# Optimization experiments

Measured on AMD Instinct MI355X. Metric: run time of the kernel, lower is better.

The kernel has to match this reference:

```python
import jax, jax.numpy as jnp
import numpy as np

B, N, DY, STD, T = 2, 8000, 12, 6, 30
DX = 0.5
DYG = 0.5
DT = 1.0

def _mlp(x, params):
    n = len(params)
    for i, (W, b) in enumerate(params):
        x = x @ W + b
        if i < n - 1:
            x = jax.nn.relu(x)
    return x

def _process_param(D, mu, coeff_vec):
    ds = DY // 3
    d33 = ds * ds
    m33 = [coeff_vec[i * d33:(i + 1) * d33].reshape(ds, ds) for i in range(4)]
    base = 4 * d33
    dd = ds * ds - ds
    diag = []
    for i in range(3):
        aij = coeff_vec[base + i * dd:base + (i + 1) * dd].reshape(ds - 1, ds)
        m = jnp.concatenate([jnp.ones((ds - 1, 1), aij.dtype), aij], axis=1).reshape(-1)
        m = jnp.concatenate([m, jnp.ones((1,), aij.dtype)]).reshape(ds, ds)
        diag.append(m)
    z = jnp.zeros((ds, ds), coeff_vec.dtype)
    rows = jnp.concatenate([
        jnp.concatenate([diag[0], z, m33[0]], axis=1),
        jnp.concatenate([z, diag[1], m33[1]], axis=1),
        jnp.concatenate([m33[2], m33[3], diag[2]], axis=1)], axis=0)
    coeffM = jax.nn.relu(rows)  # [DY, DY]
    ds0 = jnp.zeros((ds,), D.dtype)
    Dij = jax.nn.relu(jnp.concatenate([ds0, D]))  # [DY]
    MUij = jax.nn.relu(jnp.concatenate([mu[:ds], ds0, mu[-ds:]]))  # [DY]
    return coeffM, Dij, MUij

def _overlap(t, g):
    # overlap length of unit intervals centered at t and g
    omin = jax.nn.relu((t - 0.5) - (g - 0.5)) + (g - 0.5)
    omax = (t + 0.5) - jax.nn.relu((t + 0.5) - (g + 0.5))
    return jax.nn.relu(omax - omin)

def _trans_probs(dx_, dy_):
    gx, gy = jnp.meshgrid(jnp.arange(5.0), jnp.arange(5.0), indexing='ij')
    grid = jnp.stack([gx, gy], -1).reshape(25, 2)
    xl = _overlap(dx_[..., None, :], grid[:, 1].reshape(1, 1, 25, 1))
    yl = _overlap(dy_[..., None, :], grid[:, 0].reshape(1, 1, 25, 1))
    return xl * yl  # [B,N,25,C]

def _aggre(inp, a0):
    x = inp[:, a0]  # [B,N,25,C] gather
    w = jnp.concatenate([jnp.ones((1,)), jnp.full((24,), 0.01)]).reshape(1, 1, 25, 1)
    return jnp.concatenate([inp, (x * w).sum(-2)], axis=-1)

def _pde(phi, feat_dy, feat_st, D, mu, coeff_vec, trans_p, q_p, dec_p, adj4, adj25, ckpt=False):
    a4 = adj4[0]   # [N,4]
    a0 = adj25[0]  # [N,25]
    coeffM, Dij, MUij = _process_param(D, mu, coeff_vec)
    phie = phi[..., None]
    pn = phie[:, a4]  # [B,N,4,1]
    gpx = (pn[:, :, 1] - pn[:, :, 0]) / (2 * DX)
    gpy = (pn[:, :, 3] - pn[:, :, 2]) / (2 * DYG)
    phi_ag = _aggre(phie, a0)      # constant across steps
    st_ag = _aggre(feat_st, a0)    # constant across steps
    D_bn = jnp.broadcast_to(jax.lax.stop_gradient(Dij), (B, N, DY))
    MU_bn = jnp.broadcast_to(jax.lax.stop_gradient(MUij), (B, N, DY))

    def step(feat, _):
        last = feat
        fn = feat[:, a4]  # [B,N,4,C]
        J = (fn[:, :, 0] + fn[:, :, 1] - 2 * feat) / DX ** 2 + (fn[:, :, 2] + fn[:, :, 3] - 2 * feat) / DYG ** 2
        fxn = (gpx * feat)[:, a4]
        fyn = (gpy * feat)[:, a4]
        Fdiv = (fxn[:, :, 1] - fxn[:, :, 0]) / (2 * DX) + (fyn[:, :, 3] - fyn[:, :, 2]) / (2 * DYG)
        u_diff = jnp.einsum('bnc,cd->bnd', Dij * J - MUij * Fdiv, coeffM)
        mass = jnp.where(last == 0, 1.0, last)
        a_x = jnp.clip(jnp.einsum('bnc,cd->bnd', MUij * gpx, coeffM) / mass, -2.0, 2.0)
        a_y = jnp.clip(jnp.einsum('bnc,cd->bnd', MUij * gpy, coeffM) / mass, -2.0, 2.0)
        probs = _trans_probs(a_x * DT, a_y * DT)  # [B,N,25,C]
        src = probs * last[:, :, None, :]
        scat = lambda idx, s: jnp.zeros((N, DY), s.dtype).at[idx.reshape(-1)].add(s.reshape(-1, DY))
        u_rig = jax.vmap(scat)(adj25, src) - last  # scatter_add over nodes then sum over 25
        feat_tr = jnp.concatenate([_aggre(feat, a0), phi_ag, D_bn, MU_bn, st_ag], -1)  # [B,N,62]
        mix = jax.nn.sigmoid(_mlp(feat_tr, trans_p)[..., -1:])
        delta_u = mix * u_diff + (1 - mix) * u_rig
        feat_q = jnp.concatenate([_aggre(last, a0), phi_ag, st_ag], -1)  # [B,N,38]
        q0 = _mlp(feat_q, q_p)
        new = last + delta_u + q0
        fu = _mlp(jnp.concatenate([new, feat_st], -1), dec_p)  # [B,N,1]
        return new, (fu[..., 0], mix[..., 0], q0, new)

    body = jax.checkpoint(step) if ckpt else step
    _, (us_s, mix_s, q0_s, fd_s) = jax.lax.scan(body, feat_dy, None, length=T)
    us = jnp.moveaxis(us_s, 0, -1).reshape(B, N, 1, T)
    mix_m = jnp.moveaxis(mix_s, 0, -1).reshape(B, N, 1, T)
    q0_m = jnp.moveaxis(q0_s, 0, -1).reshape(B, N, DY, 1, T)
    fd = jnp.moveaxis(fd_s, 0, 2).reshape(B, N, 1, T, DY)
    return us, mix_m, q0_m, fd

def setup_inputs():
    key = jax.random.key(0)
    ks = jax.random.split(key, 24)
    def lin(k, i, o):
        kw, kb = jax.random.split(k)
        return (0.1 * jax.random.normal(kw, (i, o), jnp.float32),
                0.01 * jax.random.normal(kb, (o,), jnp.float32))
    tp = [lin(ks[0], 62, 64), lin(ks[1], 64, 32), lin(ks[2], 32, 26)]
    qp = [lin(ks[3], 38, 64), lin(ks[4], 64, 32), lin(ks[5], 32, 12)]
    dp = [lin(ks[6], 18, 32), lin(ks[7], 32, 32), lin(ks[8], 32, 64), lin(ks[9], 64, 1)]
    inp = {
        'phi': jax.random.normal(ks[10], (B, N), jnp.float32),
        'feat_dy': jax.random.uniform(ks[11], (B, N, DY), jnp.float32),
        'feat_st': jax.random.normal(ks[12], (B, N, STD), jnp.float32),
        'D': jnp.ones((2 * (DY // 3),), jnp.float32) * 0.05,
        'mu': jnp.ones((2 * (DY // 3),), jnp.float32) * 0.05,
        'coeff_vec': jnp.ones((DY * DY - 2 * (DY // 3) ** 2 - DY,), jnp.float32) * 0.05,
        'adj4': jax.random.randint(ks[13], (B, N, 4), 0, N),
        'adj25': jax.random.randint(ks[14], (B, N, 25), 0, N),
    }
    for name, p in [('trans', tp), ('q', qp), ('dec', dp)]:
        for i, (W, b) in enumerate(p):
            inp[name + '_W' + str(i)] = W
            inp[name + '_b' + str(i)] = b
    return inp

def reference(phi, feat_dy, feat_st, D, mu, coeff_vec,
              trans_W0, trans_b0, trans_W1, trans_b1, trans_W2, trans_b2,
              q_W0, q_b0, q_W1, q_b1, q_W2, q_b2,
              dec_W0, dec_b0, dec_W1, dec_b1, dec_W2, dec_b2, dec_W3, dec_b3,
              adj4, adj25):
    trans_p = [(trans_W0, trans_b0), (trans_W1, trans_b1), (trans_W2, trans_b2)]
    q_p = [(q_W0, q_b0), (q_W1, q_b1), (q_W2, q_b2)]
    dec_p = [(dec_W0, dec_b0), (dec_W1, dec_b1), (dec_W2, dec_b2), (dec_W3, dec_b3)]
    return _pde(phi, feat_dy, feat_st, D, mu, coeff_vec, trans_p, q_p, dec_p, adj4, adj25)
```

## Files before the change

### kernel.cpp

```cpp
#include <hip/hip_runtime.h>
#include <math.h>


namespace {
constexpr int NB = 2;
constexpr int NN = 8000;
constexpr int BN = NB * NN;
constexpr int TS = 30;
constexpr int CAP = 64;

constexpr int P_T0 = 0;
constexpr int P_Q0 = 1536;
constexpr int P_W1 = 3072;
constexpr int P_Q2 = 7168;
constexpr int P_Z  = 7552;
constexpr int P_D0 = 7584;
constexpr int P_D1 = 7968;
constexpr int P_D2 = 8992;
constexpr int P_D3 = 11040;
constexpr int P_BT1 = 11104;
constexpr int P_BQ1 = 11136;
constexpr int P_BQ2 = 11168;
constexpr int P_BD1 = 11184;
constexpr int P_BD2 = 11216;
constexpr int P_MISC= 11280;
constexpr int PACK_N = 11296;

constexpr int A_AG = 0;
constexpr int A_NV = 0;
constexpr int A_H1 = 24;
constexpr int A_D1 = 24;
constexpr int A_D2 = 56;
constexpr int A_H2 = 152;
constexpr int A_SLOT = 216;

constexpr int O_COEFF = 0;
constexpr int O_CFT   = 144;
constexpr int O_DIJ   = 288;
constexpr int O_MUIJ  = 300;
constexpr int O_MC    = 312;
constexpr int O_PACK  = 336;
constexpr int O_GPX   = O_PACK + PACK_N + 16;
constexpr int O_GPY   = O_GPX + BN;
constexpr int O_H1T   = O_GPY + BN;
constexpr int O_H1Q   = O_H1T + BN*64;
constexpr int O_H1D   = O_H1Q + BN*64;
constexpr int O_FEATA = O_H1D + BN*32;
constexpr int O_FEATB = O_FEATA + BN*12;
constexpr int O_AXY4A = O_FEATB + BN*12;
constexpr int O_AXY4B = O_AXY4A + BN*48;
constexpr int O_ACT   = O_AXY4B + BN*48;
constexpr int O_FLTEND= O_ACT + BN*48;
constexpr int O_STG   = O_FLTEND + BN + BN*CAP;
constexpr int STG_N = TS*BN*12;
constexpr size_t WS_NEED = (size_t)(O_STG + STG_N) * 4;

constexpr int OUS  = 0;
constexpr int OMIX = BN*TS;
constexpr int OQ0  = 2*BN*TS;
constexpr int OFD  = OQ0 + BN*12*TS;
}

__device__ __forceinline__ float group5_sum(float v, int lane) {
  int g = lane / 12, c = lane % 12;
  float s1 = __shfl(v, c + 12*((g+1)%5));
  float s2 = __shfl(v, c + 12*((g+2)%5));
  float s3 = __shfl(v, c + 12*((g+3)%5));
  float s4 = __shfl(v, c + 12*((g+4)%5));
  return v + s1 + s2 + s3 + s4;
}

__global__ void k_setup_small(const float* __restrict__ D, const float* __restrict__ mu,
                              const float* __restrict__ cv, float* ws) {
  int t = threadIdx.x;
  for (int e = t; e < 144; e += 256) {
    int r = e / 12, q = e % 12;
    int rb = r >> 2, cb = q >> 2, ri = r & 3, qi = q & 3;
    float val = 0.f;
    if (rb == cb) {
      int f = ri*4 + qi;
      if (f % 5 == 0) val = 1.f;
      else val = cv[64 + rb*12 + (f/5)*4 + (f%5) - 1];
    } else if (rb == 0 && cb == 2) val = cv[     ri*4 + qi];
    else if   (rb == 1 && cb == 2) val = cv[16 + ri*4 + qi];
    else if   (rb == 2 && cb == 0) val = cv[32 + ri*4 + qi];
    else if   (rb == 2 && cb == 1) val = cv[48 + ri*4 + qi];
    ws[O_COEFF + e] = fmaxf(val, 0.f);
  }
  if (t < 12) {
    ws[O_DIJ + t]  = (t < 4) ? 0.f : fmaxf(D[t-4], 0.f);
    ws[O_MUIJ + t] = (t < 4) ? fmaxf(mu[t], 0.f) : ((t < 8) ? 0.f : fmaxf(mu[t-4], 0.f));
  }
  __syncthreads();
  if (t < 144) {
    int r = t / 12, c = t % 12;
    ws[O_CFT + c*12 + r] = ws[O_COEFF + t];
  }
  if (t < 12) {
    float acc = 0.f;
    for (int c = 0; c < 12; c++) acc += ws[O_MUIJ + c] * ws[O_COEFF + c*12 + t];
    ws[O_MC + t] = acc;
  }
}

__global__ void k_xpose(const float* __restrict__ Wt0, const float* __restrict__ Wq0,
                        const float* __restrict__ Wt1, const float* __restrict__ Wq1,
                        const float* __restrict__ Wt2, const float* __restrict__ Wq2,
                        const float* __restrict__ Wd0, const float* __restrict__ Wd1,
                        const float* __restrict__ Wd2, const float* __restrict__ Wd3,
                        const float* __restrict__ bt1, const float* __restrict__ bq1,
                        const float* __restrict__ bt2, const float* __restrict__ bq2,
                        const float* __restrict__ bd1, const float* __restrict__ bd2,
                        const float* __restrict__ bd3,
                        float* ws) {
  const int t = blockIdx.x * blockDim.x + threadIdx.x;
  const int G = gridDim.x * blockDim.x;
  float* P = ws + O_PACK;
  for (int e = t; e < 1536; e += G) {
    int q = e / 256, r = e % 256, l = r / 4, j = r % 4;
    P[P_T0 + e] = Wt0[(4*q+j)*64 + l];
    P[P_Q0 + e] = Wq0[(4*q+j)*64 + l];
  }
  for (int e = t; e < 4096; e += G) {
    int q = e / 256, r = e % 256, l = r / 4, j = r % 4;
    P[P_W1 + e] = (l < 32) ? Wt1[(4*q+j)*32 + l] : Wq1[(4*q+j)*32 + (l-32)];
  }
  for (int e = t; e < 384; e += G) {
    int q = e / 48, r = e % 48, c = r / 4, j = r % 4;
    P[P_Q2 + e] = Wq2[(4*q+j)*12 + c];
  }
  for (int e = t; e < 32; e += G) P[P_Z + e] = Wt2[e*26 + 25];
  for (int e = t; e < 384; e += G) {
    int q = e / 128, r = e % 128, l = r / 4, j = r % 4;
    P[P_D0 + e] = Wd0[(4*q+j)*32 + l];
  }
  for (int e = t; e < 1024; e += G) {
    int q = e / 128, r = e % 128, l = r / 4, j = r % 4;
    P[P_D1 + e] = Wd1[(4*q+j)*32 + l];
  }
  for (int e = t; e < 2048; e += G) {
    int q = e / 256, r = e % 256, l = r / 4, j = r % 4;
    P[P_D2 + e] = Wd2[(4*q+j)*64 + l];
  }
  for (int e = t; e < 64; e += G) P[P_D3 + e] = Wd3[e];
  for (int e = t; e < 32; e += G) {
    P[P_BT1 + e] = bt1[e];
    P[P_BQ1 + e] = bq1[e];
    P[P_BD1 + e] = bd1[e];
  }
  for (int e = t; e < 12; e += G) P[P_BQ2 + e] = bq2[e];
  for (int e = t; e < 64; e += G) P[P_BD2 + e] = bd2[e];
  if (t == 0) { P[P_MISC + 0] = bd3[0]; P[P_MISC + 1] = bt2[25]; }
}

__global__ __launch_bounds__(256) void k_setup_node(
    const float* __restrict__ phi, const float* __restrict__ feat_dy,
    const float* __restrict__ feat_st,
    const int* __restrict__ adj4, const int* __restrict__ adj25,
    const float* __restrict__ Wt0, const float* __restrict__ bt0,
    const float* __restrict__ Wq0, const float* __restrict__ bq0,
    const float* __restrict__ Wd0, const float* __restrict__ bd0,
    float* ws, int* wsi) {
  const int wid  = (blockIdx.x * blockDim.x + threadIdx.x) >> 6;
  const int lane = threadIdx.x & 63;
  if (wid >= BN) return;
  const int b = wid / NN, n = wid % NN;

  const int* a4 = adj4 + n*4;
  const float gpx = phi[b*NN + a4[1]] - phi[b*NN + a4[0]];
  const float gpy = phi[b*NN + a4[3]] - phi[b*NN + a4[2]];
  if (lane == 0) { ws[O_GPX + wid] = gpx; ws[O_GPY + wid] = gpy; wsi[wid] = 0; }

  int idx = 0; float w = 0.f;
  if (lane < 25) { idx = adj25[n*25 + lane]; w = (lane == 0) ? 1.f : 0.01f; }
  float phiw = (lane < 25) ? w * phi[b*NN + idx] : 0.f;
  #pragma unroll
  for (int s = 32; s > 0; s >>= 1) phiw += __shfl_xor(phiw, s);

  float stv[6], stw[6];
  #pragma unroll
  for (int j = 0; j < 6; j++) {
    float x = (lane < 25) ? w * feat_st[(b*NN + idx)*6 + j] : 0.f;
    #pragma unroll
    for (int s = 32; s > 0; s >>= 1) x += __shfl_xor(x, s);
    stw[j] = x;
    stv[j] = feat_st[(b*NN + n)*6 + j];
  }
  const float phiv = phi[b*NN + n];

  float hT = bt0[lane] + phiv*Wt0[24*64 + lane] + phiw*Wt0[25*64 + lane];
  float hQ = bq0[lane] + phiv*Wq0[24*64 + lane] + phiw*Wq0[25*64 + lane];
  #pragma unroll
  for (int i = 0; i < 12; i++) {
    hT = fmaf(ws[O_DIJ  + i], Wt0[(26+i)*64 + lane], hT);
    hT = fmaf(ws[O_MUIJ + i], Wt0[(38+i)*64 + lane], hT);
  }
  #pragma unroll
  for (int j = 0; j < 6; j++) {
    hT = fmaf(stv[j], Wt0[(50+j)*64 + lane], hT);
    hT = fmaf(stw[j], Wt0[(56+j)*64 + lane], hT);
    hQ = fmaf(stv[j], Wq0[(26+j)*64 + lane], hQ);
    hQ = fmaf(stw[j], Wq0[(32+j)*64 + lane], hQ);
  }
  ws[O_H1T + wid*64 + lane] = hT;
  ws[O_H1Q + wid*64 + lane] = hQ;
  if (lane < 32) {
    float hD = bd0[lane];
    #pragma unroll
    for (int j = 0; j < 6; j++) hD = fmaf(stv[j], Wd0[(12+j)*32 + lane], hD);
    ws[O_H1D + wid*32 + lane] = hD;
  }
  if (lane < 12) {
    float f = feat_dy[wid*12 + lane];
    ws[O_FEATA + wid*12 + lane] = f;
    float mass = (f == 0.f) ? 1.f : f;
    float mc = ws[O_MC + lane];
    float axv = fminf(fmaxf(gpx*mc/mass, -2.f), 2.f);
    float ayv = fminf(fmaxf(gpy*mc/mass, -2.f), 2.f);
    float4* a4a = (float4*)(ws + O_AXY4A);
    a4a[wid*12 + lane] = make_float4(f, axv, ayv, 0.f);
  }
}

__global__ void k_build_rev(const int* __restrict__ adj25, int* wsi) {
  int i = blockIdx.x * blockDim.x + threadIdx.x;
  if (i >= BN * 25) return;
  int b = i / (NN * 25);
  int rem = i % (NN * 25);
  int m = rem / 25, k = rem % 25;
  int tgt = adj25[i];
  int slot = atomicAdd(&wsi[b*NN + tgt], 1);
  if (slot < CAP) wsi[BN + (b*NN + tgt)*CAP + slot] = (m << 5) | k;
}

__global__ __launch_bounds__(512) void k_gather(
    const float* __restrict__ ws,
    const int* __restrict__ rcnt, const int* __restrict__ rent,
    const float* __restrict__ fsrc, const float4* __restrict__ a4src,
    const int* __restrict__ adj4, const int* __restrict__ adj25,
    float* __restrict__ actb) {
  const int wid_raw = (int)((blockIdx.x * blockDim.x + threadIdx.x) >> 6);
  if (wid_raw >= BN) return;
  const int wid  = __builtin_amdgcn_readfirstlane(wid_raw);
  const int lane = threadIdx.x & 63;
  const int c12  = lane % 12;
  const int g    = lane / 12;
  const int b = wid / NN, n = wid % NN;

  const int* a4p = adj4 + n*4;
  const int m0 = a4p[0], m1 = a4p[1], m2 = a4p[2], m3 = a4p[3];
  int cnt = rcnt[wid]; if (cnt > CAP) cnt = CAP;
  const int idxv = (lane < 25) ? adj25[n*25 + lane] : 0;
  const int pkv  = rent[wid*CAP + lane];
  const float f_c  = fsrc[wid*12 + c12];
  const float dij  = ws[O_DIJ  + c12];
  const float muij = ws[O_MUIJ + c12];
  const float4* CFTp = (const float4*)(ws + O_CFT + c12*12);
  const float4 cf0 = CFTp[0], cf1 = CFTp[1], cf2 = CFTp[2];

  float agw = 0.f;
  {
    const int i0 = __shfl(idxv, g);
    const int i1 = __shfl(idxv, g + 5);
    const int i2 = __shfl(idxv, g + 10);
    const int i3 = __shfl(idxv, g + 15);
    const int i4 = __shfl(idxv, g + 20);
    if (g < 5) {
      const float v0 = fsrc[(b*NN + i0)*12 + c12];
      const float v1 = fsrc[(b*NN + i1)*12 + c12];
      const float v2 = fsrc[(b*NN + i2)*12 + c12];
      const float v3 = fsrc[(b*NN + i3)*12 + c12];
      const float v4 = fsrc[(b*NN + i4)*12 + c12];
      const float w0 = (g == 0) ? 1.f : 0.01f;
      agw = fmaf(w0,    v0, agw);
      agw = fmaf(0.01f, v1, agw);
      agw = fmaf(0.01f, v2, agw);
      agw = fmaf(0.01f, v3, agw);
      agw = fmaf(0.01f, v4, agw);
    }
    agw = group5_sum(agw, lane);
  }

  float udiff;
  {
    const float f0 = fsrc[(b*NN+m0)*12 + c12];
    const float f1 = fsrc[(b*NN+m1)*12 + c12];
    const float f2 = fsrc[(b*NN+m2)*12 + c12];
    const float f3 = fsrc[(b*NN+m3)*12 + c12];
    const float gx0 = ws[O_GPX + b*NN + m0], gx1 = ws[O_GPX + b*NN + m1];
    const float gy2 = ws[O_GPY + b*NN + m2], gy3 = ws[O_GPY + b*NN + m3];
    const float J = 4.f * ((f0+f1+f2+f3) - 4.f*f_c);
    const float Fdiv = gx1*f1 - gx0*f0 + gy3*f3 - gy2*f2;
    const float v = dij*J - muij*Fdiv;
    float acc;
    acc  = __shfl(v, 0) * cf0.x;
    acc  = fmaf(__shfl(v, 1), cf0.y, acc);
    acc  = fmaf(__shfl(v, 2), cf0.z, acc);
    acc  = fmaf(__shfl(v, 3), cf0.w, acc);
    acc  = fmaf(__shfl(v, 4), cf1.x, acc);
    acc  = fmaf(__shfl(v, 5), cf1.y, acc);
    acc  = fmaf(__shfl(v, 6), cf1.z, acc);
    acc  = fmaf(__shfl(v, 7), cf1.w, acc);
    acc  = fmaf(__shfl(v, 8), cf2.x, acc);
    acc  = fmaf(__shfl(v, 9), cf2.y, acc);
    acc  = fmaf(__shfl(v,10), cf2.z, acc);
    acc  = fmaf(__shfl(v,11), cf2.w, acc);
    udiff = acc;
  }

  float urig;
  {
    float usc = 0.f;
    #pragma unroll
    for (int it = 0; it < 8; ++it) {
      const int e = g + 5*it;
      const bool val = (g < 5) && (e < cnt);
      const int pk = __shfl(pkv, e & 63);
      const int m = pk >> 5, k = pk & 31;
      const int off = val ? ((b*NN + m)*12 + c12) : (wid*12 + c12);
      const float4 sm = a4src[off];
      const float kx = (float)(k - (k/5)*5);
      const float ky = (float)(k/5);
      const float px = fmaxf(1.f - fabsf(sm.y - kx), 0.f);
      const float py = fmaxf(1.f - fabsf(sm.z - ky), 0.f);
      usc = fmaf(val ? px*py : 0.f, sm.x, usc);
    }
    if (cnt > 40) {
      #pragma unroll
      for (int it = 8; it < 13; ++it) {
        const int e = g + 5*it;
        const bool val = (g < 5) && (e < cnt);
        const int pk = __shfl(pkv, e & 63);
        const int m = pk >> 5, k = pk & 31;
        const int off = val ? ((b*NN + m)*12 + c12) : (wid*12 + c12);
        const float4 sm = a4src[off];
        const float kx = (float)(k - (k/5)*5);
        const float ky = (float)(k/5);
        const float px = fmaxf(1.f - fabsf(sm.y - kx), 0.f);
        const float py = fmaxf(1.f - fabsf(sm.z - ky), 0.f);
        usc = fmaf(val ? px*py : 0.f, sm.x, usc);
      }
    }
    usc = group5_sum(usc, lane);
    urig = usc - f_c;
  }

  const float ov = (lane < 12) ? agw : ((lane < 24) ? udiff : urig);
  if (lane < 36) actb[wid*48 + lane] = ov;
}

__global__ __launch_bounds__(512) void k_mlp(
    const float* __restrict__ ws, const float* __restrict__ actb, int t,
    const float* __restrict__ fsrc,
    float* __restrict__ fdst, float4* __restrict__ a4dst,
    float* __restrict__ stg, int use_stage,
    float* __restrict__ out) {
  __shared__ __attribute__((aligned(16))) float sh[PACK_N + 16*A_SLOT];
  const int tid = threadIdx.x;
  {
    const float4* wp = (const float4*)(ws + O_PACK);
    float4* sp = (float4*)sh;
    for (int e = tid; e < PACK_N/4; e += 512) sp[e] = wp[e];
  }
  __syncthreads();

  const int wv   = tid >> 6;
  const int wvq  = __builtin_amdgcn_readfirstlane(wv);
  const int lane = tid & 63;
  const int c12 = lane % 12;
  const int l32 = lane & 31;
  const bool isQ = lane >= 32;
  float* act0 = sh + PACK_N + (wvq*2 + 0)*A_SLOT;
  float* act1 = sh + PACK_N + (wvq*2 + 1)*A_SLOT;

  const float mcv = ws[O_MC + c12];

  #pragma unroll 1
  for (int pass = 0; pass < 2; pass++) {
    const int nb = (blockIdx.x*16 + pass*8 + wvq) * 2;

    float f_c[2], udiff[2], urig[2];
    #pragma unroll
    for (int j = 0; j < 2; j++) {
      const int wid = nb + j;
      float* actj = j ? act1 : act0;
      f_c[j] = fsrc[wid*12 + c12];
      const float agv = actb[wid*48 + c12];
      udiff[j] = actb[wid*48 + 12 + c12];
      urig[j]  = actb[wid*48 + 24 + c12];
      if (lane < 24) actj[A_AG + lane] = (lane < 12) ? f_c[j] : agv;
    }

    {
      float h1t0 = ws[O_H1T + nb*64 + lane];
      float h1q0 = ws[O_H1Q + nb*64 + lane];
      float h1t1 = ws[O_H1T + (nb+1)*64 + lane];
      float h1q1 = ws[O_H1Q + (nb+1)*64 + lane];
      #pragma unroll
      for (int q = 0; q < 6; q++) {
        const float4 wt = *(const float4*)&sh[P_T0 + q*256 + lane*4];
        const float4 wq = *(const float4*)&sh[P_Q0 + q*256 + lane*4];
        const float4 a0 = *(const float4*)&act0[A_AG + 4*q];
        const float4 a1 = *(const float4*)&act1[A_AG + 4*q];
        h1t0 = fmaf(a0.x, wt.x, h1t0); h1q0 = fmaf(a0.x, wq.x, h1q0);
        h1t0 = fmaf(a0.y, wt.y, h1t0); h1q0 = fmaf(a0.y, wq.y, h1q0);
        h1t0 = fmaf(a0.z, wt.z, h1t0); h1q0 = fmaf(a0.z, wq.z, h1q0);
        h1t0 = fmaf(a0.w, wt.w, h1t0); h1q0 = fmaf(a0.w, wq.w, h1q0);
        h1t1 = fmaf(a1.x, wt.x, h1t1); h1q1 = fmaf(a1.x, wq.x, h1q1);
        h1t1 = fmaf(a1.y, wt.y, h1t1); h1q1 = fmaf(a1.y, wq.y, h1q1);
        h1t1 = fmaf(a1.z, wt.z, h1t1); h1q1 = fmaf(a1.z, wq.z, h1q1);
        h1t1 = fmaf(a1.w, wt.w, h1t1); h1q1 = fmaf(a1.w, wq.w, h1q1);
      }
      act0[A_H1 + lane]      = fmaxf(h1t0, 0.f);
      act0[A_H1 + 64 + lane] = fmaxf(h1q0, 0.f);
      act1[A_H1 + lane]      = fmaxf(h1t1, 0.f);
      act1[A_H1 + 64 + lane] = fmaxf(h1q1, 0.f);
    }

    {
      const int hoff = isQ ? 64 : 0;
      float h2_0 = isQ ? sh[P_BQ1 + l32] : sh[P_BT1 + l32];
      float h2_1 = h2_0;
      #pragma unroll
      for (int q = 0; q < 16; q++) {
        const float4 w  = *(const float4*)&sh[P_W1 + q*256 + lane*4];
        const float4 a0 = *(const float4*)&act0[A_H1 + hoff + 4*q];
        const float4 a1 = *(const float4*)&act1[A_H1 + hoff + 4*q];
        h2_0 = fmaf(a0.x, w.x, h2_0); h2_1 = fmaf(a1.x, w.x, h2_1);
        h2_0 = fmaf(a0.y, w.y, h2_0); h2_1 = fmaf(a1.y, w.y, h2_1);
        h2_0 = fmaf(a0.z, w.z, h2_0); h2_1 = fmaf(a1.z, w.z, h2_1);
        h2_0 = fmaf(a0.w, w.w, h2_0); h2_1 = fmaf(a1.w, w.w, h2_1);
      }
      act0[A_H2 + lane] = fmaxf(h2_0, 0.f);
      act1[A_H2 + lane] = fmaxf(h2_1, 0.f);
    }

    float mix[2], q0v[2];
    {
      float mz0 = sh[P_MISC + 1], mz1 = mz0;
      float q00 = sh[P_BQ2 + c12], q01 = q00;
      #pragma unroll
      for (int q = 0; q < 8; q++) {
        const float4 wz  = *(const float4*)&sh[P_Z + 4*q];
        const float4 wq  = *(const float4*)&sh[P_Q2 + q*48 + c12*4];
        const float4 at0 = *(const float4*)&act0[A_H2 + 4*q];
        const float4 aq0 = *(const float4*)&act0[A_H2 + 32 + 4*q];
        const float4 at1 = *(const float4*)&act1[A_H2 + 4*q];
        const float4 aq1 = *(const float4*)&act1[A_H2 + 32 + 4*q];
        mz0 = fmaf(at0.x, wz.x, mz0); q00 = fmaf(aq0.x, wq.x, q00);
        mz0 = fmaf(at0.y, wz.y, mz0); q00 = fmaf(aq0.y, wq.y, q00);
        mz0 = fmaf(at0.z, wz.z, mz0); q00 = fmaf(aq0.z, wq.z, q00);
        mz0 = fmaf(at0.w, wz.w, mz0); q00 = fmaf(aq0.w, wq.w, q00);
        mz1 = fmaf(at1.x, wz.x, mz1); q01 = fmaf(aq1.x, wq.x, q01);
        mz1 = fmaf(at1.y, wz.y, mz1); q01 = fmaf(aq1.y, wq.y, q01);
        mz1 = fmaf(at1.z, wz.z, mz1); q01 = fmaf(aq1.z, wq.z, q01);
        mz1 = fmaf(at1.w, wz.w, mz1); q01 = fmaf(aq1.w, wq.w, q01);
      }
      mix[0] = 1.f / (1.f + expf(-mz0));
      mix[1] = 1.f / (1.f + expf(-mz1));
      q0v[0] = q00; q0v[1] = q01;
    }

    #pragma unroll
    for (int j = 0; j < 2; j++) {
      const int wid = nb + j;
      float* actj = j ? act1 : act0;
      const float newv = f_c[j] + mix[j]*udiff[j] + (1.f - mix[j])*urig[j] + q0v[j];
      if (lane < 12) {
        actj[A_NV + lane] = newv;
        if (use_stage) stg[(size_t)t*BN*12 + wid*12 + lane] = q0v[j];
        else           out[OQ0 + (wid*12 + lane)*TS + t] = q0v[j];
        out[OFD + (wid*TS + t)*12 + lane] = newv;
        fdst[wid*12 + lane] = newv;
        float mass = (newv == 0.f) ? 1.f : newv;
        float gpxn = ws[O_GPX + wid], gpyn = ws[O_GPY + wid];
        float axn = fminf(fmaxf(gpxn*mcv/mass, -2.f), 2.f);
        float ayn = fminf(fmaxf(gpyn*mcv/mass, -2.f), 2.f);
        a4dst[wid*12 + lane] = make_float4(newv, axn, ayn, 0.f);
      }
      if (lane == 0) out[OMIX + wid*TS + t] = mix[j];
    }

    {
      float d1_0 = ws[O_H1D + nb*32 + l32];
      float d1_1 = ws[O_H1D + (nb+1)*32 + l32];
      #pragma unroll
      for (int q = 0; q < 3; q++) {
        const float4 w  = *(const float4*)&sh[P_D0 + q*128 + l32*4];
        const float4 a0 = *(const float4*)&act0[A_NV + 4*q];
        const float4 a1 = *(const float4*)&act1[A_NV + 4*q];
        d1_0 = fmaf(a0.x, w.x, d1_0); d1_1 = fmaf(a1.x, w.x, d1_1);
        d1_0 = fmaf(a0.y, w.y, d1_0); d1_1 = fmaf(a1.y, w.y, d1_1);
        d1_0 = fmaf(a0.z, w.z, d1_0); d1_1 = fmaf(a1.z, w.z, d1_1);
        d1_0 = fmaf(a0.w, w.w, d1_0); d1_1 = fmaf(a1.w, w.w, d1_1);
      }
      if (lane < 32) {
        act0[A_D1 + lane] = fmaxf(d1_0, 0.f);
        act1[A_D1 + lane] = fmaxf(d1_1, 0.f);
      }
    }
    {
      float d2_0 = sh[P_BD1 + l32], d2_1 = d2_0;
      #pragma unroll
      for (int q = 0; q < 8; q++) {
        const float4 w  = *(const float4*)&sh[P_D1 + q*128 + l32*4];
        const float4 a0 = *(const float4*)&act0[A_D1 + 4*q];
        const float4 a1 = *(const float4*)&act1[A_D1 + 4*q];
        d2_0 = fmaf(a0.x, w.x, d2_0); d2_1 = fmaf(a1.x, w.x, d2_1);
        d2_0 = fmaf(a0.y, w.y, d2_0); d2_1 = fmaf(a1.y, w.y, d2_1);
        d2_0 = fmaf(a0.z, w.z, d2_0); d2_1 = fmaf(a1.z, w.z, d2_1);
        d2_0 = fmaf(a0.w, w.w, d2_0); d2_1 = fmaf(a1.w, w.w, d2_1);
      }
      if (lane < 32) {
        act0[A_D2 + lane] = fmaxf(d2_0, 0.f);
        act1[A_D2 + lane] = fmaxf(d2_1, 0.f);
      }
    }
    {
      float d3_0 = sh[P_BD2 + lane], d3_1 = d3_0;
      #pragma unroll
      for (int q = 0; q < 8; q++) {
        const float4 w  = *(const float4*)&sh[P_D2 + q*256 + lane*4];
        const float4 a0 = *(const float4*)&act0[A_D2 + 4*q];
        const float4 a1 = *(const float4*)&act1[A_D2 + 4*q];
        d3_0 = fmaf(a0.x, w.x, d3_0); d3_1 = fmaf(a1.x, w.x, d3_1);
        d3_0 = fmaf(a0.y, w.y, d3_0); d3_1 = fmaf(a1.y, w.y, d3_1);
        d3_0 = fmaf(a0.z, w.z, d3_0); d3_1 = fmaf(a1.z, w.z, d3_1);
        d3_0 = fmaf(a0.w, w.w, d3_0); d3_1 = fmaf(a1.w, w.w, d3_1);
      }
      const float wd3 = sh[P_D3 + lane];
      float u0 = fmaxf(d3_0, 0.f) * wd3;
      float u1 = fmaxf(d3_1, 0.f) * wd3;
      #pragma unroll
      for (int s2 = 32; s2 > 0; s2 >>= 1) {
        u0 += __shfl_xor(u0, s2);
        u1 += __shfl_xor(u1, s2);
      }
      if (lane == 0) {
        const float b3 = sh[P_MISC + 0];
        out[OUS + nb*TS + t]     = u0 + b3;
        out[OUS + (nb+1)*TS + t] = u1 + b3;
      }
    }
  }
}

__global__ void k_out(const float* __restrict__ stg, float* __restrict__ out) {
  const size_t NQ = (size_t)BN*12*TS;
  size_t i = (size_t)blockIdx.x * blockDim.x + threadIdx.x;
  if (i < NQ) {
    int e = (int)(i / TS), t = (int)(i % TS);
    out[OQ0 + i] = stg[(size_t)t*BN*12 + e];
  }
}

extern "C" void kernel_launch(void* const* d_in, const int* in_sizes, int n_in,
                              void* d_out, int out_size, void* d_ws, size_t ws_size,
                              hipStream_t stream) {
  const float* phi     = (const float*)d_in[0];
  const float* feat_dy = (const float*)d_in[1];
  const float* feat_st = (const float*)d_in[2];
  const float* Dv      = (const float*)d_in[3];
  const float* muv     = (const float*)d_in[4];
  const float* cv      = (const float*)d_in[5];
  const int*   adj4    = (const int*)d_in[6];
  const int*   adj25   = (const int*)d_in[7];
  const float* Wt0 = (const float*)d_in[8];
  const float* bt0 = (const float*)d_in[9];
  const float* Wt1 = (const float*)d_in[10];
  const float* bt1 = (const float*)d_in[11];
  const float* Wt2 = (const float*)d_in[12];
  const float* bt2 = (const float*)d_in[13];
  const float* Wq0 = (const float*)d_in[14];
  const float* bq0 = (const float*)d_in[15];
  const float* Wq1 = (const float*)d_in[16];
  const float* bq1 = (const float*)d_in[17];
  const float* Wq2 = (const float*)d_in[18];
  const float* bq2 = (const float*)d_in[19];
  const float* Wd0 = (const float*)d_in[20];
  const float* bd0 = (const float*)d_in[21];
  const float* Wd1 = (const float*)d_in[22];
  const float* bd1 = (const float*)d_in[23];
  const float* Wd2 = (const float*)d_in[24];
  const float* bd2 = (const float*)d_in[25];
  const float* Wd3 = (const float*)d_in[26];
  const float* bd3 = (const float*)d_in[27];

  float* ws  = (float*)d_ws;
  int*   wsi = (int*)(ws + O_FLTEND);
  float* out = (float*)d_out;
  const int use_stage = (ws_size >= WS_NEED) ? 1 : 0;
  float* stg = ws + O_STG;
  float* actb = ws + O_ACT;

  k_setup_small<<<1, 256, 0, stream>>>(Dv, muv, cv, ws);
  k_xpose<<<16, 256, 0, stream>>>(Wt0, Wq0, Wt1, Wq1, Wt2, Wq2, Wd0, Wd1, Wd2, Wd3,
                                  bt1, bq1, bt2, bq2, bd1, bd2, bd3, ws);
  k_setup_node<<<BN/4, 256, 0, stream>>>(phi, feat_dy, feat_st, adj4, adj25,
                                         Wt0, bt0, Wq0, bq0, Wd0, bd0, ws, wsi);
  k_build_rev<<<(BN*25 + 255)/256, 256, 0, stream>>>(adj25, wsi);

  float* fa = ws + O_FEATA; float* fb = ws + O_FEATB;
  float4* pa = (float4*)(ws + O_AXY4A);
  float4* pb = (float4*)(ws + O_AXY4B);
  for (int t = 0; t < TS; t++) {
    k_gather<<<BN/8, 512, 0, stream>>>(ws, wsi, wsi + BN, fa, pa, adj4, adj25, actb);
    k_mlp<<<BN/32, 512, 0, stream>>>(ws, actb, t, fa, fb, pb, stg, use_stage, out);
    float* tf = fa; fa = fb; fb = tf;
    float4* tp = pa; pa = pb; pb = tp;
  }
  if (use_stage) {
    const size_t tot = (size_t)BN*12*TS;
    k_out<<<(unsigned)((tot + 255)/256), 256, 0, stream>>>(stg, out);
  }
}
```

Measured before the change: 1.271 ms.

## Fuse per-step gather and MLP kernels, passing activations through shared memory

Merges the per-timestep gather kernel into the MLP kernel. Each wave now gathers four nodes, overlapping the global gathers with the weight copy into LDS, and writes its 36 activations to shared memory instead of a global buffer. This removes one launch per timestep and the global round trip of the activation buffer. In exchange, each wave does four times the gather work serially, so there is less gather parallelism and higher register and LDS use (launch bounds 512,4).

```diff
diff --git a/kernel.cpp b/kernel.cpp
--- a/kernel.cpp
+++ b/kernel.cpp
@@ -34,6 +34,9 @@
 constexpr int A_H2 = 152;
 constexpr int A_SLOT = 216;
 
+constexpr int G_ACT  = PACK_N + 16*A_SLOT;
+constexpr int SH_N   = G_ACT + 32*36;
+
 constexpr int O_COEFF = 0;
 constexpr int O_CFT   = 144;
 constexpr int O_DIJ   = 288;
@@ -49,8 +52,7 @@
 constexpr int O_FEATB = O_FEATA + BN*12;
 constexpr int O_AXY4A = O_FEATB + BN*12;
 constexpr int O_AXY4B = O_AXY4A + BN*48;
-constexpr int O_ACT   = O_AXY4B + BN*48;
-constexpr int O_FLTEND= O_ACT + BN*48;
+constexpr int O_FLTEND= O_AXY4B + BN*48;
 constexpr int O_STG   = O_FLTEND + BN + BN*CAP;
 constexpr int STG_N = TS*BN*12;
 constexpr size_t WS_NEED = (size_t)(O_STG + STG_N) * 4;
@@ -233,151 +235,163 @@
   if (slot < CAP) wsi[BN + (b*NN + tgt)*CAP + slot] = (m << 5) | k;
 }
 
-__global__ __launch_bounds__(512) void k_gather(
+__global__ __launch_bounds__(512, 4) void k_step2(
     const float* __restrict__ ws,
-    const int* __restrict__ rcnt, const int* __restrict__ rent,
+    const int* __restrict__ rcnt, const int* __restrict__ rent, int t,
     const float* __restrict__ fsrc, const float4* __restrict__ a4src,
+    float* __restrict__ fdst, float4* __restrict__ a4dst,
     const int* __restrict__ adj4, const int* __restrict__ adj25,
-    float* __restrict__ actb) {
-  const int wid_raw = (int)((blockIdx.x * blockDim.x + threadIdx.x) >> 6);
-  if (wid_raw >= BN) return;
-  const int wid  = __builtin_amdgcn_readfirstlane(wid_raw);
-  const int lane = threadIdx.x & 63;
-  const int c12  = lane % 12;
-  const int g    = lane / 12;
-  const int b = wid / NN, n = wid % NN;
-
-  const int* a4p = adj4 + n*4;
-  const int m0 = a4p[0], m1 = a4p[1], m2 = a4p[2], m3 = a4p[3];
-  int cnt = rcnt[wid]; if (cnt > CAP) cnt = CAP;
-  const int idxv = (lane < 25) ? adj25[n*25 + lane] : 0;
-  const int pkv  = rent[wid*CAP + lane];
-  const float f_c  = fsrc[wid*12 + c12];
-  const float dij  = ws[O_DIJ  + c12];
-  const float muij = ws[O_MUIJ + c12];
-  const float4* CFTp = (const float4*)(ws + O_CFT + c12*12);
-  const float4 cf0 = CFTp[0], cf1 = CFTp[1], cf2 = CFTp[2];
-
-  float agw = 0.f;
-  {
-    const int i0 = __shfl(idxv, g);
-    const int i1 = __shfl(idxv, g + 5);
-    const int i2 = __shfl(idxv, g + 10);
-    const int i3 = __shfl(idxv, g + 15);
-    const int i4 = __shfl(idxv, g + 20);
-    if (g < 5) {
-      const float v0 = fsrc[(b*NN + i0)*12 + c12];
-      const float v1 = fsrc[(b*NN + i1)*12 + c12];
-      const float v2 = fsrc[(b*NN + i2)*12 + c12];
-      const float v3 = fsrc[(b*NN + i3)*12 + c12];
-      const float v4 = fsrc[(b*NN + i4)*12 + c12];
-      const float w0 = (g == 0) ? 1.f : 0.01f;
-      agw = fmaf(w0,    v0, agw);
-      agw = fmaf(0.01f, v1, agw);
-      agw = fmaf(0.01f, v2, agw);
-      agw = fmaf(0.01f, v3, agw);
-      agw = fmaf(0.01f, v4, agw);
-    }
-    agw = group5_sum(agw, lane);
-  }
-
-  float udiff;
-  {
-    const float f0 = fsrc[(b*NN+m0)*12 + c12];
-    const float f1 = fsrc[(b*NN+m1)*12 + c12];
-    const float f2 = fsrc[(b*NN+m2)*12 + c12];
-    const float f3 = fsrc[(b*NN+m3)*12 + c12];
-    const float gx0 = ws[O_GPX + b*NN + m0], gx1 = ws[O_GPX + b*NN + m1];
-    const float gy2 = ws[O_GPY + b*NN + m2], gy3 = ws[O_GPY + b*NN + m3];
-    const float J = 4.f * ((f0+f1+f2+f3) - 4.f*f_c);
-    const float Fdiv = gx1*f1 - gx0*f0 + gy3*f3 - gy2*f2;
-    const float v = dij*J - muij*Fdiv;
-    float acc;
-    acc  = __shfl(v, 0) * cf0.x;
-    acc  = fmaf(__shfl(v, 1), cf0.y, acc);
-    acc  = fmaf(__shfl(v, 2), cf0.z, acc);
-    acc  = fmaf(__shfl(v, 3), cf0.w, acc);
-    acc  = fmaf(__shfl(v, 4), cf1.x, acc);
-    acc  = fmaf(__shfl(v, 5), cf1.y, acc);
-    acc  = fmaf(__shfl(v, 6), cf1.z, acc);
-    acc  = fmaf(__shfl(v, 7), cf1.w, acc);
-    acc  = fmaf(__shfl(v, 8), cf2.x, acc);
-    acc  = fmaf(__shfl(v, 9), cf2.y, acc);
-    acc  = fmaf(__shfl(v,10), cf2.z, acc);
-    acc  = fmaf(__shfl(v,11), cf2.w, acc);
-    udiff = acc;
-  }
-
-  float urig;
-  {
-    float usc = 0.f;
-    #pragma unroll
-    for (int it = 0; it < 8; ++it) {
-      const int e = g + 5*it;
-      const bool val = (g < 5) && (e < cnt);
-      const int pk = __shfl(pkv, e & 63);
-      const int m = pk >> 5, k = pk & 31;
-      const int off = val ? ((b*NN + m)*12 + c12) : (wid*12 + c12);
-      const float4 sm = a4src[off];
-      const float kx = (float)(k - (k/5)*5);
-      const float ky = (float)(k/5);
-      const float px = fmaxf(1.f - fabsf(sm.y - kx), 0.f);
-      const float py = fmaxf(1.f - fabsf(sm.z - ky), 0.f);
-      usc = fmaf(val ? px*py : 0.f, sm.x, usc);
-    }
-    if (cnt > 40) {
-      #pragma unroll
-      for (int it = 8; it < 13; ++it) {
-        const int e = g + 5*it;
-        const bool val = (g < 5) && (e < cnt);
-        const int pk = __shfl(pkv, e & 63);
-        const int m = pk >> 5, k = pk & 31;
-        const int off = val ? ((b*NN + m)*12 + c12) : (wid*12 + c12);
-        const float4 sm = a4src[off];
-        const float kx = (float)(k - (k/5)*5);
-        const float ky = (float)(k/5);
-        const float px = fmaxf(1.f - fabsf(sm.y - kx), 0.f);
-        const float py = fmaxf(1.f - fabsf(sm.z - ky), 0.f);
-        usc = fmaf(val ? px*py : 0.f, sm.x, usc);
-      }
-    }
-    usc = group5_sum(usc, lane);
-    urig = usc - f_c;
-  }
-
-  const float ov = (lane < 12) ? agw : ((lane < 24) ? udiff : urig);
-  if (lane < 36) actb[wid*48 + lane] = ov;
-}
-
-__global__ __launch_bounds__(512) void k_mlp(
-    const float* __restrict__ ws, const float* __restrict__ actb, int t,
-    const float* __restrict__ fsrc,
-    float* __restrict__ fdst, float4* __restrict__ a4dst,
     float* __restrict__ stg, int use_stage,
     float* __restrict__ out) {
-  __shared__ __attribute__((aligned(16))) float sh[PACK_N + 16*A_SLOT];
+  __shared__ __attribute__((aligned(16))) float sh[SH_N];
   const int tid = threadIdx.x;
   {
     const float4* wp = (const float4*)(ws + O_PACK);
     float4* sp = (float4*)sh;
     for (int e = tid; e < PACK_N/4; e += 512) sp[e] = wp[e];
   }
-  __syncthreads();
 
   const int wv   = tid >> 6;
   const int wvq  = __builtin_amdgcn_readfirstlane(wv);
   const int lane = tid & 63;
   const int c12 = lane % 12;
+  const int g   = lane / 12;
   const int l32 = lane & 31;
   const bool isQ = lane >= 32;
+
+  {
+    const int nbase = blockIdx.x*32 + wvq*4;
+    const int b = nbase / NN;
+    const float dij  = ws[O_DIJ  + c12];
+    const float muij = ws[O_MUIJ + c12];
+    const float4* CFTp = (const float4*)(ws + O_CFT + c12*12);
+    const float4 cf0 = CFTp[0], cf1 = CFTp[1], cf2 = CFTp[2];
+
+    int idxv4[4], pkv4[4], cnt4[4];
+    float fc4[4];
+    int ms0[4], ms1[4], ms2[4], ms3[4];
+    #pragma unroll
+    for (int i = 0; i < 4; i++) {
+      const int wid = nbase + i;
+      const int n = wid - b*NN;
+      idxv4[i] = (lane < 25) ? adj25[n*25 + lane] : 0;
+      pkv4[i]  = rent[wid*CAP + lane];
+      int c = rcnt[wid]; cnt4[i] = (c > CAP) ? CAP : c;
+      fc4[i]   = fsrc[wid*12 + c12];
+      const int* a4p = adj4 + n*4;
+      ms0[i] = a4p[0]; ms1[i] = a4p[1]; ms2[i] = a4p[2]; ms3[i] = a4p[3];
+    }
+
+    #pragma unroll
+    for (int i = 0; i < 4; i++) {
+      const int wid = nbase + i;
+      const float f_c = fc4[i];
+      const int cnt = cnt4[i];
+      const int idxv = idxv4[i];
+      const int pkv = pkv4[i];
+      const int m0 = ms0[i], m1 = ms1[i], m2 = ms2[i], m3 = ms3[i];
+
+      float agw = 0.f;
+      {
+        const int i0 = __shfl(idxv, g);
+        const int i1 = __shfl(idxv, g + 5);
+        const int i2 = __shfl(idxv, g + 10);
+        const int i3 = __shfl(idxv, g + 15);
+        const int i4 = __shfl(idxv, g + 20);
+        if (g < 5) {
+          const float v0 = fsrc[(b*NN + i0)*12 + c12];
+          const float v1 = fsrc[(b*NN + i1)*12 + c12];
+          const float v2 = fsrc[(b*NN + i2)*12 + c12];
+          const float v3 = fsrc[(b*NN + i3)*12 + c12];
+          const float v4 = fsrc[(b*NN + i4)*12 + c12];
+          const float w0 = (g == 0) ? 1.f : 0.01f;
+          agw = fmaf(w0,    v0, agw);
+          agw = fmaf(0.01f, v1, agw);
+          agw = fmaf(0.01f, v2, agw);
+          agw = fmaf(0.01f, v3, agw);
+          agw = fmaf(0.01f, v4, agw);
+        }
+        agw = group5_sum(agw, lane);
+      }
+
+      float udiff;
+      {
+        const float f0 = fsrc[(b*NN+m0)*12 + c12];
+        const float f1 = fsrc[(b*NN+m1)*12 + c12];
+        const float f2 = fsrc[(b*NN+m2)*12 + c12];
+        const float f3 = fsrc[(b*NN+m3)*12 + c12];
+        const float gx0 = ws[O_GPX + b*NN + m0], gx1 = ws[O_GPX + b*NN + m1];
+        const float gy2 = ws[O_GPY + b*NN + m2], gy3 = ws[O_GPY + b*NN + m3];
+        const float J = 4.f * ((f0+f1+f2+f3) - 4.f*f_c);
+        const float Fdiv = gx1*f1 - gx0*f0 + gy3*f3 - gy2*f2;
+        const float v = dij*J - muij*Fdiv;
+        float acc;
+        acc  = __shfl(v, 0) * cf0.x;
+        acc  = fmaf(__shfl(v, 1), cf0.y, acc);
+        acc  = fmaf(__shfl(v, 2), cf0.z, acc);
+        acc  = fmaf(__shfl(v, 3), cf0.w, acc);
+        acc  = fmaf(__shfl(v, 4), cf1.x, acc);
+        acc  = fmaf(__shfl(v, 5), cf1.y, acc);
+        acc  = fmaf(__shfl(v, 6), cf1.z, acc);
+        acc  = fmaf(__shfl(v, 7), cf1.w, acc);
+        acc  = fmaf(__shfl(v, 8), cf2.x, acc);
+        acc  = fmaf(__shfl(v, 9), cf2.y, acc);
+        acc  = fmaf(__shfl(v,10), cf2.z, acc);
+        acc  = fmaf(__shfl(v,11), cf2.w, acc);
+        udiff = acc;
+      }
+
+      float urig;
+      {
+        float usc = 0.f;
+        #pragma unroll
+        for (int it = 0; it < 8; ++it) {
+          const int e = g + 5*it;
+          const bool val = (g < 5) && (e < cnt);
+          const int pk = __shfl(pkv, e & 63);
+          const int m = pk >> 5, k = pk & 31;
+          const int off = val ? ((b*NN + m)*12 + c12) : (wid*12 + c12);
+          const float4 sm = a4src[off];
+          const float kx = (float)(k - (k/5)*5);
+          const float ky = (float)(k/5);
+          const float px = fmaxf(1.f - fabsf(sm.y - kx), 0.f);
+          const float py = fmaxf(1.f - fabsf(sm.z - ky), 0.f);
+          usc = fmaf(val ? px*py : 0.f, sm.x, usc);
+        }
+        if (cnt > 40) {
+          #pragma unroll
+          for (int it = 8; it < 13; ++it) {
+            const int e = g + 5*it;
+            const bool val = (g < 5) && (e < cnt);
+            const int pk = __shfl(pkv, e & 63);
+            const int m = pk >> 5, k = pk & 31;
+            const int off = val ? ((b*NN + m)*12 + c12) : (wid*12 + c12);
+            const float4 sm = a4src[off];
+            const float kx = (float)(k - (k/5)*5);
+            const float ky = (float)(k/5);
+            const float px = fmaxf(1.f - fabsf(sm.y - kx), 0.f);
+            const float py = fmaxf(1.f - fabsf(sm.z - ky), 0.f);
+            usc = fmaf(val ? px*py : 0.f, sm.x, usc);
+          }
+        }
+        usc = group5_sum(usc, lane);
+        urig = usc - f_c;
+      }
+
+      const float ov = (lane < 12) ? agw : ((lane < 24) ? udiff : urig);
+      if (lane < 36) sh[G_ACT + (wvq*4 + i)*36 + lane] = ov;
+    }
+  }
+  __syncthreads();
+
   float* act0 = sh + PACK_N + (wvq*2 + 0)*A_SLOT;
   float* act1 = sh + PACK_N + (wvq*2 + 1)*A_SLOT;
-
   const float mcv = ws[O_MC + c12];
 
   #pragma unroll 1
   for (int pass = 0; pass < 2; pass++) {
-    const int nb = (blockIdx.x*16 + pass*8 + wvq) * 2;
+    const int lnb = (pass*8 + wvq)*2;
+    const int nb  = blockIdx.x*32 + lnb;
 
     float f_c[2], udiff[2], urig[2];
     #pragma unroll
@@ -385,9 +399,9 @@
       const int wid = nb + j;
       float* actj = j ? act1 : act0;
       f_c[j] = fsrc[wid*12 + c12];
-      const float agv = actb[wid*48 + c12];
-      udiff[j] = actb[wid*48 + 12 + c12];
-      urig[j]  = actb[wid*48 + 24 + c12];
+      const float agv = sh[G_ACT + (lnb+j)*36 + c12];
+      udiff[j] = sh[G_ACT + (lnb+j)*36 + 12 + c12];
+      urig[j]  = sh[G_ACT + (lnb+j)*36 + 24 + c12];
       if (lane < 24) actj[A_AG + lane] = (lane < 12) ? f_c[j] : agv;
     }
 
@@ -591,7 +605,6 @@
   float* out = (float*)d_out;
   const int use_stage = (ws_size >= WS_NEED) ? 1 : 0;
   float* stg = ws + O_STG;
-  float* actb = ws + O_ACT;
 
   k_setup_small<<<1, 256, 0, stream>>>(Dv, muv, cv, ws);
   k_xpose<<<16, 256, 0, stream>>>(Wt0, Wq0, Wt1, Wq1, Wt2, Wq2, Wd0, Wd1, Wd2, Wd3,
@@ -604,8 +617,8 @@
   float4* pa = (float4*)(ws + O_AXY4A);
   float4* pb = (float4*)(ws + O_AXY4B);
   for (int t = 0; t < TS; t++) {
-    k_gather<<<BN/8, 512, 0, stream>>>(ws, wsi, wsi + BN, fa, pa, adj4, adj25, actb);
-    k_mlp<<<BN/32, 512, 0, stream>>>(ws, actb, t, fa, fb, pb, stg, use_stage, out);
+    k_step2<<<BN/32, 512, 0, stream>>>(ws, wsi, wsi + BN, t, fa, pa, fb, pb,
+                                       adj4, adj25, stg, use_stage, out);
     float* tf = fa; fa = fb; fb = tf;
     float4* tp = pa; pa = pb; pb = tp;
   }
```

New measurement: 1.644 ms. +29.3%, slower.
